# Optimization experiments

Measured on AMD Instinct MI355X. Metric: run time of the kernel, lower is better.

Reference implementation:

```python
import jax, jax.numpy as jnp
import numpy as np

B, S, E, H, W, L = 2048, 50, 256, 512, 256, 50  # batch, seq, emb, hidden, weight, answer_seq_len
V = 50 + 1  # input_size + 1 embedding rows


def _uni(k, shape, bound):
    return jax.random.uniform(k, shape, jnp.float32, -bound, bound)


def setup_inputs() -> dict:
    key = jax.random.key(0)
    ks = jax.random.split(key, 14)
    kb = 1.0 / np.sqrt(H)  # torch LSTM/Linear init bound 1/sqrt(hidden)
    inp = {
        'input': jax.random.randint(ks[0], (B, S), 0, V),
        'emb': jax.random.normal(ks[1], (V, E), jnp.float32),
        'enc_Wih': _uni(ks[2], (4 * H, E), kb),
        'enc_Whh': _uni(ks[3], (4 * H, H), kb),
        'enc_bih': _uni(ks[4], (4 * H,), kb),
        'enc_bhh': _uni(ks[5], (4 * H,), kb),
        'dec_Wih': _uni(ks[6], (4 * H, E), kb),
        'dec_Whh': _uni(ks[7], (4 * H, H), kb),
        'dec_bih': _uni(ks[8], (4 * H,), kb),
        'dec_bhh': _uni(ks[9], (4 * H,), kb),
        'W1': _uni(ks[10], (W, H), kb),
        'W2': _uni(ks[11], (W, H), kb),
        'vt': _uni(ks[12], (W,), 1.0 / np.sqrt(W)),
    }
    return inp


def _lstm_cell(x, h, c, Wih, Whh, bih, bhh):
    gates = x @ Wih.T + h @ Whh.T + (bih + bhh)
    i, f, g, o = jnp.split(gates, 4, axis=-1)  # torch gate order i,f,g,o
    c = jax.nn.sigmoid(f) * c + jax.nn.sigmoid(i) * jnp.tanh(g)
    h = jax.nn.sigmoid(o) * jnp.tanh(c)
    return h, c


def reference(input, emb, enc_Wih, enc_Whh, enc_bih, enc_bhh,
              dec_Wih, dec_Whh, dec_bih, dec_bhh, W1, W2, vt):
    x = emb[input]  # [B,S,E]

    def enc_step(carry, xt):
        h, c = carry
        h, c = _lstm_cell(xt, h, c, enc_Wih, enc_Whh, enc_bih, enc_bhh)
        return (h, c), h

    z = jnp.zeros((B, H), x.dtype)
    _, enc_seq = jax.lax.scan(enc_step, (z, z), x.transpose(1, 0, 2))  # [S,B,H]
    enc_states = enc_seq.transpose(1, 0, 2)  # [B,S,H]

    # W1(encoder_states) is loop-invariant; compute once (same math as per-step recompute)
    blend1 = jnp.einsum('bsh,wh->bsw', enc_states, W1)  # [B,S,W]

    dec_in = jnp.zeros((B, E), x.dtype)  # original never updates decoder_input
    h0 = jnp.zeros((B, H), x.dtype)
    c0 = enc_seq[-1]  # cell_state = encoder_states[-1]
    mask0 = jnp.zeros((B, S), bool)

    def dec_step(carry, k):
        h, c, mask = carry
        h, c = _lstm_cell(dec_in, h, c, dec_Wih, dec_Whh, dec_bih, dec_bhh)
        blend2 = h @ W2.T  # [B,W]
        scores = jnp.einsum('bsw,w->bs', jnp.tanh(blend1 + blend2[:, None, :]), vt)
        scores = jnp.where(mask, jnp.float32(-100000.0), scores)
        logp = jax.nn.log_softmax(scores, axis=-1)  # [B,S]
        chosen = jax.random.categorical(k, logp, axis=-1)  # [B]
        mask = mask.at[jnp.arange(B), chosen].set(True)
        return (h, c, mask), (logp, chosen)

    keys = jax.random.split(jax.random.key(42), L)
    _, (probs, tour) = jax.lax.scan(dec_step, (h0, c0, mask0), keys)
    probs = probs.transpose(1, 0, 2)  # [B,L,S]
    tour = tour.transpose(1, 0)       # [B,L]
    return probs, tour
```

## Files before the change

kernel.cpp:

```cpp
#include <hip/hip_runtime.h>
#include <cstdint>

#define Bsz 2048
#define Ssz 50
#define Esz 256
#define Hsz 512
#define Wsz 256
#define Lsz 50
#define Vsz 51
#define KI 16
#define CH 10
#define GFRAGC2 ((size_t)32 * 128 * 512)

#define JAX_THREEFRY_PARTITIONABLE 1

typedef _Float16 f16;
typedef _Float16 f16x8 __attribute__((ext_vector_type(8)));
typedef float f32x4 __attribute__((ext_vector_type(4)));

__host__ __device__ __forceinline__ void threefry2x32_hd(
    unsigned k0, unsigned k1, unsigned x0, unsigned x1,
    unsigned& o0, unsigned& o1) {
  unsigned ks2 = k0 ^ k1 ^ 0x1BD11BDAu;
  x0 += k0; x1 += k1;
#define TF_RND(r) { x0 += x1; x1 = (x1 << (r)) | (x1 >> (32 - (r))); x1 ^= x0; }
  TF_RND(13) TF_RND(15) TF_RND(26) TF_RND(6)
  x0 += k1; x1 += ks2 + 1u;
  TF_RND(17) TF_RND(29) TF_RND(16) TF_RND(24)
  x0 += ks2; x1 += k0 + 2u;
  TF_RND(13) TF_RND(15) TF_RND(26) TF_RND(6)
  x0 += k0; x1 += k1 + 3u;
  TF_RND(17) TF_RND(29) TF_RND(16) TF_RND(24)
  x0 += k1; x1 += ks2 + 4u;
  TF_RND(13) TF_RND(15) TF_RND(26) TF_RND(6)
  x0 += ks2; x1 += k0 + 5u;
#undef TF_RND
  o0 = x0; o1 = x1;
}

__global__ __launch_bounds__(512) void prep_gfrag(const float* __restrict__ Whh,
                                                  f16* __restrict__ dst) {
  int blk = blockIdx.x;
  int ntile = blk >> 5, kc = blk & 31;
  int t = threadIdx.x;
  int l = t >> 3, e = t & 7;
  int c = l & 15, kg = l >> 4;
  int n = ntile * 16 + c;
  int k = (kc & 15) * 32 + kg * 8 + e;
  int j = n >> 2, g = n & 3;
  float w = Whh[(size_t)(g * 512 + j) * 512 + k];
  f16 hi = (f16)w;
  float lo = w - (float)hi;
  f16 val = (kc < 16) ? hi : (f16)(lo * 2048.0f);
  dst[((size_t)kc * 128 + ntile) * 512 + t] = val;
}

__global__ __launch_bounds__(512) void prep_bfrag(const float* __restrict__ Wm,
                                                  f16* __restrict__ dst) {
  int blk = blockIdx.x;
  int wtile = blk >> 5, kc = blk & 31;
  int t = threadIdx.x;
  int l = t >> 3, e = t & 7;
  int c = l & 15, kg = l >> 4;
  int n = wtile * 16 + c;
  int k = (kc & 15) * 32 + kg * 8 + e;
  float w = Wm[(size_t)n * 512 + k];
  f16 hi = (f16)w;
  float lo = w - (float)hi;
  f16 val = (kc < 16) ? hi : (f16)(lo * 2048.0f);
  dst[((size_t)kc * 16 + wtile) * 512 + t] = val;
}

__global__ __launch_bounds__(256) void prep_encin(
    const float* __restrict__ emb, const float* __restrict__ Wih,
    const float* __restrict__ bih, const float* __restrict__ bhh,
    float* __restrict__ encInP) {
  int wid = blockIdx.x * 4 + (threadIdx.x >> 6);
  int lane = threadIdx.x & 63;
  if (wid >= Vsz * 2048) return;
  int v = wid >> 11, col = wid & 2047;
  float4 e = ((const float4*)emb)[v * 64 + lane];
  float4 w = ((const float4*)Wih)[col * 64 + lane];
  float d = e.x * w.x + e.y * w.y + e.z * w.z + e.w * w.w;
  for (int off = 32; off; off >>= 1) d += __shfl_xor(d, off);
  if (lane == 0) {
    int g = col >> 9, j = col & 511;
    encInP[(size_t)v * 2048 + j * 4 + g] = d + bih[col] + bhh[col];
  }
}

__global__ __launch_bounds__(256) void prep_dbias(const float* __restrict__ a,
                                                  const float* __restrict__ b,
                                                  float* __restrict__ dst) {
  int col = blockIdx.x * 256 + threadIdx.x;
  int g = col >> 9, j = col & 511;
  dst[j * 4 + g] = a[col] + b[col];
}

__global__ __launch_bounds__(256, 2) void gates_mfma(
    const f16* __restrict__ Afrag,
    const f16* __restrict__ Bfrag,
    const float* __restrict__ addtab, const int* __restrict__ input, int tstep,
    f16* __restrict__ Aout,
    float* __restrict__ cio) {
  __shared__ float Cst[64][132];
  const int t = threadIdx.x;
  const int lane = t & 63;
  const int wid = t >> 6;
  const int wm = wid >> 1, wn = wid & 1;
  const int bid = blockIdx.x;
  const int xcd = bid & 7, loc = bid >> 3;
  const int mblk = xcd * 4 + (loc >> 4);
  const int nblk = loc & 15;

  const f16* Ab = Afrag + (size_t)(mblk * 4 + wm * 2) * 512 + lane * 8;
  const f16* Bb = Bfrag + (size_t)(nblk * 8 + wn * 4) * 512 + lane * 8;

  f32x4 acc1[2][4], acc2[2][4];
  {
    f32x4 z = {0.f, 0.f, 0.f, 0.f};
#pragma unroll
    for (int i = 0; i < 2; ++i)
#pragma unroll
      for (int j = 0; j < 4; ++j) { acc1[i][j] = z; acc2[i][j] = z; }
  }

  f16x8 pah[2], pal[2], pbh[4], pbl[4];
  f16x8 qah[2], qal[2], qbh[4], qbl[4];

#define GLOAD(AH_, AL_, BH_, BL_, ki_)                                        \
  {                                                                           \
    const f16* ak = Ab + (size_t)(ki_)*65536;                                 \
    const f16* bk = Bb + (size_t)(ki_)*65536;                                 \
    _Pragma("unroll")                                                         \
    for (int q = 0; q < 2; ++q) {                                             \
      AH_[q] = *(const f16x8*)(ak + q * 512);                                 \
      AL_[q] = *(const f16x8*)(ak + (size_t)16 * 65536 + q * 512);            \
    }                                                                         \
    _Pragma("unroll")                                                         \
    for (int q = 0; q < 4; ++q) {                                             \
      BH_[q] = *(const f16x8*)(bk + q * 512);                                 \
      BL_[q] = *(const f16x8*)(bk + (size_t)16 * 65536 + q * 512);            \
    }                                                                         \
  }
#define GMM(AH_, AL_, BH_, BL_)                                               \
  {                                                                           \
    _Pragma("unroll")                                                         \
    for (int mt = 0; mt < 2; ++mt)                                            \
      _Pragma("unroll")                                                       \
      for (int nt = 0; nt < 4; ++nt)                                          \
        acc1[mt][nt] = __builtin_amdgcn_mfma_f32_16x16x32_f16(                \
            AH_[mt], BH_[nt], acc1[mt][nt], 0, 0, 0);                         \
    _Pragma("unroll")                                                         \
    for (int mt = 0; mt < 2; ++mt)                                            \
      _Pragma("unroll")                                                       \
      for (int nt = 0; nt < 4; ++nt)                                          \
        acc1[mt][nt] = __builtin_amdgcn_mfma_f32_16x16x32_f16(                \
            AL_[mt], BH_[nt], acc1[mt][nt], 0, 0, 0);                         \
    _Pragma("unroll")                                                         \
    for (int mt = 0; mt < 2; ++mt)                                            \
      _Pragma("unroll")                                                       \
      for (int nt = 0; nt < 4; ++nt)                                          \
        acc2[mt][nt] = __builtin_amdgcn_mfma_f32_16x16x32_f16(                \
            AH_[mt], BL_[nt], acc2[mt][nt], 0, 0, 0);                         \
  }

  GLOAD(pah, pal, pbh, pbl, 0)
#pragma unroll 1
  for (int ki = 0; ki < KI; ki += 2) {
    GLOAD(qah, qal, qbh, qbl, ki + 1)
    GMM(pah, pal, pbh, pbl)
    if (ki + 2 < KI) GLOAD(pah, pal, pbh, pbl, ki + 2)
    GMM(qah, qal, qbh, qbl)
  }
#undef GLOAD
#undef GMM

#pragma unroll
  for (int mt = 0; mt < 2; ++mt)
#pragma unroll
    for (int nt = 0; nt < 4; ++nt)
#pragma unroll
      for (int rg = 0; rg < 4; ++rg)
        Cst[wm * 32 + mt * 16 + (lane >> 4) * 4 + rg]
           [wn * 64 + nt * 16 + (lane & 15)] =
            acc1[mt][nt][rg] + acc2[mt][nt][rg] * (1.0f / 2048.0f);
  __syncthreads();

  const int bloc = t & 63, jg = t >> 6;
  const int bg = mblk * 64 + bloc;
  const float* arow = input
      ? addtab + (size_t)input[(size_t)bg * Ssz + tstep] * 2048
      : addtab;

  const int j0 = nblk * 32 + jg * 8;
  float* cp = cio + (size_t)bg * 512 + j0;
  float4 cv0 = *(const float4*)(cp);
  float4 cv1 = *(const float4*)(cp + 4);
  float cin[8] = {cv0.x, cv0.y, cv0.z, cv0.w, cv1.x, cv1.y, cv1.z, cv1.w};
  float cn[8], hv[8];
#pragma unroll
  for (int jj = 0; jj < 8; ++jj) {
    float4 gq = *(const float4*)(&Cst[bloc][jg * 32 + jj * 4]);
    float4 av = *(const float4*)(arow + (size_t)(j0 + jj) * 4);
    float gi = gq.x + av.x;
    float gf = gq.y + av.y;
    float gg = gq.z + av.z;
    float go = gq.w + av.w;
    float si = 1.0f / (1.0f + expf(-gi));
    float sf = 1.0f / (1.0f + expf(-gf));
    float sg = tanhf(gg);
    float so = 1.0f / (1.0f + expf(-go));
    float c2 = sf * cin[jj] + si * sg;
    cn[jj] = c2;
    hv[jj] = so * tanhf(c2);
  }
  *(float4*)(cp)     = make_float4(cn[0], cn[1], cn[2], cn[3]);
  *(float4*)(cp + 4) = make_float4(cn[4], cn[5], cn[6], cn[7]);

  f16x8 hi8, lo8;
#pragma unroll
  for (int jj = 0; jj < 8; ++jj) {
    f16 hi = (f16)hv[jj];
    hi8[jj] = hi;
    lo8[jj] = (f16)(hv[jj] - (float)hi);
  }
  const int kcH = j0 >> 5;
  const int kg = (j0 >> 3) & 3;
  size_t base = (((size_t)kcH * 128 + (bg >> 4)) * 64 + kg * 16 + (bg & 15)) * 8;
  *(f16x8*)(Aout + base)                       = hi8;
  *(f16x8*)(Aout + base + (size_t)16 * 65536)  = lo8;
}

__global__ __launch_bounds__(256) void blend_big(
    const f16* __restrict__ hChunk, const f16* __restrict__ Wb,
    float* __restrict__ outBase, int stepStride, int rowStride) {
  const int t = threadIdx.x, lane = t & 63, wid = t >> 6;
  const int wm = wid >> 1, wn = wid & 1;
  const int bid = blockIdx.x;
  const int xcd = bid & 7;
  const int r1 = bid >> 3;
  const int nblk = r1 & 7;
  const int r2 = r1 >> 3;
  const int mrem = r2 & 3;
  const int s = r2 >> 2;
  const int mblkL = xcd * 4 + mrem;
  const f16* Ab = hChunk + (size_t)s * GFRAGC2
                + (size_t)(mblkL * 4 + wm * 2) * 512 + lane * 8;
  const f16* Bb = Wb + (size_t)(nblk * 2 + wn) * 512 + lane * 8;

  f32x4 acc1[2], acc2[2];
  {
    f32x4 z = {0.f, 0.f, 0.f, 0.f};
    acc1[0] = z; acc1[1] = z; acc2[0] = z; acc2[1] = z;
  }
  f16x8 pah[2], pal[2], pbh, pbl, qah[2], qal[2], qbh, qbl;

#define BLOAD(AH_, AL_, BH_, BL_, ki_)                                        \
  {                                                                           \
    const f16* ak = Ab + (size_t)(ki_)*65536;                                 \
    const f16* bk = Bb + (size_t)(ki_)*8192;                                  \
    _Pragma("unroll")                                                         \
    for (int q = 0; q < 2; ++q) {                                             \
      AH_[q] = *(const f16x8*)(ak + q * 512);                                 \
      AL_[q] = *(const f16x8*)(ak + (size_t)16 * 65536 + q * 512);            \
    }                                                                         \
    BH_ = *(const f16x8*)(bk);                                                \
    BL_ = *(const f16x8*)(bk + (size_t)16 * 8192);                            \
  }
#define BMM(AH_, AL_, BH_, BL_)                                               \
  {                                                                           \
    _Pragma("unroll")                                                         \
    for (int mt = 0; mt < 2; ++mt)                                            \
      acc1[mt] = __builtin_amdgcn_mfma_f32_16x16x32_f16(                      \
          AH_[mt], BH_, acc1[mt], 0, 0, 0);                                   \
    _Pragma("unroll")                                                         \
    for (int mt = 0; mt < 2; ++mt)                                            \
      acc1[mt] = __builtin_amdgcn_mfma_f32_16x16x32_f16(                      \
          AL_[mt], BH_, acc1[mt], 0, 0, 0);                                   \
    _Pragma("unroll")                                                         \
    for (int mt = 0; mt < 2; ++mt)                                            \
      acc2[mt] = __builtin_amdgcn_mfma_f32_16x16x32_f16(                      \
          AH_[mt], BL_, acc2[mt], 0, 0, 0);                                   \
  }

  BLOAD(pah, pal, pbh, pbl, 0)
#pragma unroll 1
  for (int ki = 0; ki < KI; ki += 2) {
    BLOAD(qah, qal, qbh, qbl, ki + 1)
    BMM(pah, pal, pbh, pbl)
    if (ki + 2 < KI) BLOAD(pah, pal, pbh, pbl, ki + 2)
    BMM(qah, qal, qbh, qbl)
  }
#undef BLOAD
#undef BMM

  const int r = lane & 15, rg4 = (lane >> 4) * 4;
  float* ob = outBase + (size_t)s * stepStride;
#pragma unroll
  for (int mt = 0; mt < 2; ++mt)
#pragma unroll
    for (int rg = 0; rg < 4; ++rg) {
      int b = mblkL * 64 + wm * 32 + mt * 16 + rg4 + rg;
      int w = nblk * 32 + wn * 16 + r;
      float val = acc1[mt][rg] + acc2[mt][rg] * (1.0f / 2048.0f);
      ob[(size_t)b * rowStride + w] = __expf(2.0f * val);
    }
}

__global__ __launch_bounds__(256) void dec_cinit(const f16* __restrict__ hE,
                                                 float* __restrict__ cD) {
  int idx = blockIdx.x * 256 + threadIdx.x;
  int b = idx >> 9, j = idx & 511;
  size_t base = (((size_t)(j >> 5) * 128 + (b >> 4)) * 64
                 + ((j >> 3) & 3) * 16 + (b & 15)) * 8 + (j & 7);
  cD[idx] = (float)hE[base] + (float)hE[base + (size_t)16 * 65536];
}

__global__ __launch_bounds__(512) void sample_chunk(
    const float* __restrict__ b1, const float* __restrict__ b2c,
    const float* __restrict__ vt, unsigned long long* __restrict__ mask,
    float* __restrict__ probs, float* __restrict__ tour, int k0) {
  __shared__ float e1s[Ssz * Wsz];
  __shared__ float scbuf[2][52];
  const int t = threadIdx.x, b = blockIdx.x;
  const int wid = t >> 6, lane = t & 63;
  {
    const float4* src = (const float4*)(b1 + (size_t)b * Ssz * Wsz);
    for (int i = t; i < (Ssz * Wsz) / 4; i += 512)
      ((float4*)e1s)[i] = src[i];
  }
  const float vtr0 = vt[lane], vtr1 = vt[lane + 64];
  const float vtr2 = vt[lane + 128], vtr3 = vt[lane + 192];
  unsigned long long m = (wid == 7) ? mask[b] : 0ull;
  __syncthreads();

#define SCORE_ROWS(step_, dst_)                                               \
  {                                                                           \
    const float* b2p = b2c + ((size_t)(step_) * Bsz + b) * Wsz;               \
    float e20 = b2p[lane];                                                    \
    float e21 = b2p[lane + 64];                                               \
    float e22 = b2p[lane + 128];                                              \
    float e23 = b2p[lane + 192];                                              \
    for (int s = wid; s < Ssz; s += 7) {                                      \
      const float* row = e1s + s * Wsz;                                       \
      float r0 = __frcp_rn(fmaf(row[lane], e20, 1.0f));                       \
      float v = vtr0 * fmaf(-2.0f, r0, 1.0f);                                 \
      float r1 = __frcp_rn(fmaf(row[lane + 64], e21, 1.0f));                  \
      v += vtr1 * fmaf(-2.0f, r1, 1.0f);                                      \
      float r2 = __frcp_rn(fmaf(row[lane + 128], e22, 1.0f));                 \
      v += vtr2 * fmaf(-2.0f, r2, 1.0f);                                      \
      float r3 = __frcp_rn(fmaf(row[lane + 192], e23, 1.0f));                 \
      v += vtr3 * fmaf(-2.0f, r3, 1.0f);                                      \
      for (int off = 32; off; off >>= 1) v += __shfl_xor(v, off);             \
      if (lane == 0) (dst_)[s] = v;                                           \
    }                                                                         \
  }

  if (wid < 7) SCORE_ROWS(0, scbuf[0])
  __syncthreads();

#pragma unroll 1
  for (int kk = 0; kk < CH; ++kk) {
    if (wid < 7) {
      if (kk + 1 < CH) SCORE_ROWS(kk + 1, scbuf[(kk + 1) & 1])
    } else {
      const float* sc = scbuf[kk & 1];
      const int stepk = k0 + kk;
      float x = (lane < Ssz) ? sc[lane] : -INFINITY;
      if (lane < Ssz && ((m >> lane) & 1ull)) x = -100000.0f;
      float mv = x;
      for (int off = 32; off; off >>= 1) mv = fmaxf(mv, __shfl_xor(mv, off));
      float sh = x - mv;
      float e = (lane < Ssz) ? expf(sh) : 0.f;
      float ssum = e;
      for (int off = 32; off; off >>= 1) ssum += __shfl_xor(ssum, off);
      float lg = logf(ssum);
      float logp = sh - lg;
      if (lane < Ssz) probs[(size_t)b * (Lsz * Ssz) + stepk * Ssz + lane] = logp;

      unsigned kA, kB;
#if JAX_THREEFRY_PARTITIONABLE
      threefry2x32_hd(0u, 42u, 0u, (unsigned)stepk, kA, kB);
#else
      {
        unsigned a0, a1, c0, c1;
        int k = stepk;
        if (k < 25) {
          threefry2x32_hd(0u, 42u, 2u * k,      2u * k + 50u, a0, a1); kA = a0;
          threefry2x32_hd(0u, 42u, 2u * k + 1u, 2u * k + 51u, c0, c1); kB = c0;
        } else {
          threefry2x32_hd(0u, 42u, 2u * k - 50u, 2u * k,      a0, a1); kA = a1;
          threefry2x32_hd(0u, 42u, 2u * k - 49u, 2u * k + 1u, c0, c1); kB = c1;
        }
      }
#endif
      float val = -INFINITY;
      if (lane < Ssz) {
        unsigned j = (unsigned)(b * Ssz + lane);
        unsigned o0, o1, bits;
#if JAX_THREEFRY_PARTITIONABLE
        threefry2x32_hd(kA, kB, 0u, j, o0, o1);
        bits = o0 ^ o1;
#else
        if (j < 51200u) { threefry2x32_hd(kA, kB, j, j + 51200u, o0, o1); bits = o0; }
        else           { threefry2x32_hd(kA, kB, j - 51200u, j, o0, o1); bits = o1; }
#endif
        float f = __uint_as_float((bits >> 9) | 0x3F800000u) - 1.0f;
        float u = fmaxf(1.17549435e-38f, f + 1.17549435e-38f);
        val = logp - logf(-logf(u));
      }
      int idx = lane;
      for (int off = 32; off; off >>= 1) {
        float ov = __shfl_xor(val, off);
        int oi = __shfl_xor(idx, off);
        if (ov > val || (ov == val && oi < idx)) { val = ov; idx = oi; }
      }
      if (lane == 0) tour[(size_t)b * Lsz + stepk] = (float)idx;
      m |= (1ull << idx);
    }
    __syncthreads();
  }
#undef SCORE_ROWS
  if (wid == 7 && lane == 0) mask[b] = m;
}

extern "C" void kernel_launch(void* const* d_in, const int* in_sizes, int n_in,
                              void* d_out, int out_size, void* d_ws, size_t ws_size,
                              hipStream_t stream) {
  (void)in_sizes; (void)n_in; (void)out_size; (void)ws_size;
  const int*   input = (const int*)d_in[0];
  const float* emb   = (const float*)d_in[1];
  const float* eWih  = (const float*)d_in[2];
  const float* eWhh  = (const float*)d_in[3];
  const float* ebih  = (const float*)d_in[4];
  const float* ebhh  = (const float*)d_in[5];
  const float* dWhh  = (const float*)d_in[7];
  const float* dbih  = (const float*)d_in[8];
  const float* dbhh  = (const float*)d_in[9];
  const float* W1    = (const float*)d_in[10];
  const float* W2    = (const float*)d_in[11];
  const float* vt    = (const float*)d_in[12];
  float* outF = (float*)d_out;

  float* wsf = (float*)d_ws;
  size_t o = 0;
  const size_t BFRAG = (size_t)32 * 16 * 512;
  f16* BfE = (f16*)(wsf + o); o += GFRAGC2 / 2;
  f16* BfD = (f16*)(wsf + o); o += GFRAGC2 / 2;
  f16* Bb1 = (f16*)(wsf + o); o += BFRAG / 2;
  f16* Bb2 = (f16*)(wsf + o); o += BFRAG / 2;
  float* encInP = wsf + o; o += (size_t)Vsz * 2048;
  float* dbiasP = wsf + o; o += 2048;
  f16* hZero = (f16*)(wsf + o); o += GFRAGC2 / 2;
  f16* hBuf  = (f16*)(wsf + o); o += CH * (GFRAGC2 / 2);
  float* cE  = wsf + o; o += (size_t)Bsz * Hsz;
  float* b2c = wsf + o; o += (size_t)CH * Bsz * Wsz;
  float* b1  = wsf + o; o += (size_t)Bsz * Ssz * Wsz;
  unsigned long long* maskp = (unsigned long long*)(wsf + o); o += Bsz * 2;

  hipMemsetAsync(hZero, 0, GFRAGC2 * 2, stream);
  hipMemsetAsync(cE, 0, (size_t)Bsz * Hsz * 4, stream);
  hipMemsetAsync(maskp, 0, (size_t)Bsz * 8, stream);

  prep_gfrag<<<128 * 32, 512, 0, stream>>>(eWhh, BfE);
  prep_gfrag<<<128 * 32, 512, 0, stream>>>(dWhh, BfD);
  prep_bfrag<<<16 * 32, 512, 0, stream>>>(W1, Bb1);
  prep_bfrag<<<16 * 32, 512, 0, stream>>>(W2, Bb2);
  prep_encin<<<(Vsz * 2048) / 4, 256, 0, stream>>>(emb, eWih, ebih, ebhh, encInP);
  prep_dbias<<<8, 256, 0, stream>>>(dbih, dbhh, dbiasP);

  const size_t GF = GFRAGC2;

  for (int c = 0; c < Ssz / CH; ++c) {
    for (int s = 0; s < CH; ++s) {
      int t = c * CH + s;
      const f16* in = (t == 0) ? hZero : hBuf + (size_t)((t - 1) % CH) * GF;
      gates_mfma<<<512, 256, 0, stream>>>(in, BfE, encInP, input, t,
                                          hBuf + (size_t)s * GF, cE);
    }
    blend_big<<<8 * 8 * 4 * CH, 256, 0, stream>>>(hBuf, Bb1,
                                                  b1 + (size_t)(c * CH) * Wsz,
                                                  Wsz, Ssz * Wsz);
  }
  dec_cinit<<<(Bsz * Hsz) / 256, 256, 0, stream>>>(
      hBuf + (size_t)((Ssz - 1) % CH) * GF, cE);

  for (int c = 0; c < Lsz / CH; ++c) {
    for (int s = 0; s < CH; ++s) {
      int k = c * CH + s;
      const f16* in = (k == 0) ? hZero : hBuf + (size_t)((k - 1) % CH) * GF;
      gates_mfma<<<512, 256, 0, stream>>>(in, BfD, dbiasP, nullptr, 0,
                                          hBuf + (size_t)s * GF, cE);
    }
    blend_big<<<8 * 8 * 4 * CH, 256, 0, stream>>>(hBuf, Bb2, b2c,
                                                  Bsz * Wsz, Wsz);
    sample_chunk<<<Bsz, 512, 0, stream>>>(b1, b2c, vt, maskp, outF,
                                          outF + (size_t)Bsz * Lsz * Ssz,
                                          c * CH);
  }
}
```

Baseline: 3.289 ms.

## Fuse per-chunk LSTM gate steps into one persistent kernel with grid barrier

The ten per-step gates_mfma launches in each chunk become a single gates_chain launch. That kernel loops over the steps and synchronises all 512 blocks through a global atomic counter with spin-wait after each step. The counter is zeroed once and counts up across the encoder and decoder steps. The aim is to remove kernel launch and drain overhead between dependent recurrent steps, at the cost of a software grid barrier. This relies on all 512 blocks being co-resident, since the launch bounds allow two per CU, and it could deadlock if they are not.

```diff
diff --git a/kernel.cpp b/kernel.cpp
--- a/kernel.cpp
+++ b/kernel.cpp
@@ -97,12 +97,14 @@
   dst[j * 4 + g] = a[col] + b[col];
 }
 
-__global__ __launch_bounds__(256, 2) void gates_mfma(
-    const f16* __restrict__ Afrag,
+__global__ __launch_bounds__(256, 2) void gates_chain(
+    const f16* __restrict__ hIn0,
+    f16* __restrict__ hBuf,
     const f16* __restrict__ Bfrag,
-    const float* __restrict__ addtab, const int* __restrict__ input, int tstep,
-    f16* __restrict__ Aout,
-    float* __restrict__ cio) {
+    const float* __restrict__ addtab, const int* __restrict__ input,
+    int t0, int tzero,
+    float* __restrict__ cio,
+    unsigned* __restrict__ ctr) {
   __shared__ float Cst[64][132];
   const int t = threadIdx.x;
   const int lane = t & 63;
@@ -113,20 +115,27 @@
   const int mblk = xcd * 4 + (loc >> 4);
   const int nblk = loc & 15;
 
-  const f16* Ab = Afrag + (size_t)(mblk * 4 + wm * 2) * 512 + lane * 8;
+  const size_t aoff = (size_t)(mblk * 4 + wm * 2) * 512 + lane * 8;
   const f16* Bb = Bfrag + (size_t)(nblk * 8 + wn * 4) * 512 + lane * 8;
 
-  f32x4 acc1[2][4], acc2[2][4];
-  {
-    f32x4 z = {0.f, 0.f, 0.f, 0.f};
-#pragma unroll
-    for (int i = 0; i < 2; ++i)
-#pragma unroll
-      for (int j = 0; j < 4; ++j) { acc1[i][j] = z; acc2[i][j] = z; }
-  }
-
-  f16x8 pah[2], pal[2], pbh[4], pbl[4];
-  f16x8 qah[2], qal[2], qbh[4], qbl[4];
+#pragma unroll 1
+  for (int s = 0; s < CH; ++s) {
+    const int tstep = t0 + s;
+    const f16* Ab = ((tstep == tzero)
+                     ? hIn0 : hBuf + (size_t)((tstep - 1) % CH) * GFRAGC2) + aoff;
+    f16* Aout = hBuf + (size_t)(tstep % CH) * GFRAGC2;
+
+    f32x4 acc1[2][4], acc2[2][4];
+    {
+      f32x4 z = {0.f, 0.f, 0.f, 0.f};
+#pragma unroll
+      for (int i = 0; i < 2; ++i)
+#pragma unroll
+        for (int j = 0; j < 4; ++j) { acc1[i][j] = z; acc2[i][j] = z; }
+    }
+
+    f16x8 pah[2], pal[2], pbh[4], pbl[4];
+    f16x8 qah[2], qal[2], qbh[4], qbl[4];
 
 #define GLOAD(AH_, AL_, BH_, BL_, ki_)                                        \
   {                                                                           \
@@ -165,71 +174,85 @@
             AH_[mt], BL_[nt], acc2[mt][nt], 0, 0, 0);                         \
   }
 
-  GLOAD(pah, pal, pbh, pbl, 0)
+    GLOAD(pah, pal, pbh, pbl, 0)
 #pragma unroll 1
-  for (int ki = 0; ki < KI; ki += 2) {
-    GLOAD(qah, qal, qbh, qbl, ki + 1)
-    GMM(pah, pal, pbh, pbl)
-    if (ki + 2 < KI) GLOAD(pah, pal, pbh, pbl, ki + 2)
-    GMM(qah, qal, qbh, qbl)
-  }
+    for (int ki = 0; ki < KI; ki += 2) {
+      GLOAD(qah, qal, qbh, qbl, ki + 1)
+      GMM(pah, pal, pbh, pbl)
+      if (ki + 2 < KI) GLOAD(pah, pal, pbh, pbl, ki + 2)
+      GMM(qah, qal, qbh, qbl)
+    }
 #undef GLOAD
 #undef GMM
 
-#pragma unroll
-  for (int mt = 0; mt < 2; ++mt)
-#pragma unroll
-    for (int nt = 0; nt < 4; ++nt)
-#pragma unroll
-      for (int rg = 0; rg < 4; ++rg)
-        Cst[wm * 32 + mt * 16 + (lane >> 4) * 4 + rg]
-           [wn * 64 + nt * 16 + (lane & 15)] =
-            acc1[mt][nt][rg] + acc2[mt][nt][rg] * (1.0f / 2048.0f);
-  __syncthreads();
-
-  const int bloc = t & 63, jg = t >> 6;
-  const int bg = mblk * 64 + bloc;
-  const float* arow = input
-      ? addtab + (size_t)input[(size_t)bg * Ssz + tstep] * 2048
-      : addtab;
-
-  const int j0 = nblk * 32 + jg * 8;
-  float* cp = cio + (size_t)bg * 512 + j0;
-  float4 cv0 = *(const float4*)(cp);
-  float4 cv1 = *(const float4*)(cp + 4);
-  float cin[8] = {cv0.x, cv0.y, cv0.z, cv0.w, cv1.x, cv1.y, cv1.z, cv1.w};
-  float cn[8], hv[8];
-#pragma unroll
-  for (int jj = 0; jj < 8; ++jj) {
-    float4 gq = *(const float4*)(&Cst[bloc][jg * 32 + jj * 4]);
-    float4 av = *(const float4*)(arow + (size_t)(j0 + jj) * 4);
-    float gi = gq.x + av.x;
-    float gf = gq.y + av.y;
-    float gg = gq.z + av.z;
-    float go = gq.w + av.w;
-    float si = 1.0f / (1.0f + expf(-gi));
-    float sf = 1.0f / (1.0f + expf(-gf));
-    float sg = tanhf(gg);
-    float so = 1.0f / (1.0f + expf(-go));
-    float c2 = sf * cin[jj] + si * sg;
-    cn[jj] = c2;
-    hv[jj] = so * tanhf(c2);
-  }
-  *(float4*)(cp)     = make_float4(cn[0], cn[1], cn[2], cn[3]);
-  *(float4*)(cp + 4) = make_float4(cn[4], cn[5], cn[6], cn[7]);
-
-  f16x8 hi8, lo8;
-#pragma unroll
-  for (int jj = 0; jj < 8; ++jj) {
-    f16 hi = (f16)hv[jj];
-    hi8[jj] = hi;
-    lo8[jj] = (f16)(hv[jj] - (float)hi);
-  }
-  const int kcH = j0 >> 5;
-  const int kg = (j0 >> 3) & 3;
-  size_t base = (((size_t)kcH * 128 + (bg >> 4)) * 64 + kg * 16 + (bg & 15)) * 8;
-  *(f16x8*)(Aout + base)                       = hi8;
-  *(f16x8*)(Aout + base + (size_t)16 * 65536)  = lo8;
+    __syncthreads();
+#pragma unroll
+    for (int mt = 0; mt < 2; ++mt)
+#pragma unroll
+      for (int nt = 0; nt < 4; ++nt)
+#pragma unroll
+        for (int rg = 0; rg < 4; ++rg)
+          Cst[wm * 32 + mt * 16 + (lane >> 4) * 4 + rg]
+             [wn * 64 + nt * 16 + (lane & 15)] =
+              acc1[mt][nt][rg] + acc2[mt][nt][rg] * (1.0f / 2048.0f);
+    __syncthreads();
+
+    const int bloc = t & 63, jg = t >> 6;
+    const int bg = mblk * 64 + bloc;
+    const float* arow = input
+        ? addtab + (size_t)input[(size_t)bg * Ssz + tstep] * 2048
+        : addtab;
+
+    const int j0 = nblk * 32 + jg * 8;
+    float* cp = cio + (size_t)bg * 512 + j0;
+    float4 cv0 = *(const float4*)(cp);
+    float4 cv1 = *(const float4*)(cp + 4);
+    float cin[8] = {cv0.x, cv0.y, cv0.z, cv0.w, cv1.x, cv1.y, cv1.z, cv1.w};
+    float cn[8], hv[8];
+#pragma unroll
+    for (int jj = 0; jj < 8; ++jj) {
+      float4 gq = *(const float4*)(&Cst[bloc][jg * 32 + jj * 4]);
+      float4 av = *(const float4*)(arow + (size_t)(j0 + jj) * 4);
+      float gi = gq.x + av.x;
+      float gf = gq.y + av.y;
+      float gg = gq.z + av.z;
+      float go = gq.w + av.w;
+      float si = 1.0f / (1.0f + expf(-gi));
+      float sf = 1.0f / (1.0f + expf(-gf));
+      float sg = tanhf(gg);
+      float so = 1.0f / (1.0f + expf(-go));
+      float c2 = sf * cin[jj] + si * sg;
+      cn[jj] = c2;
+      hv[jj] = so * tanhf(c2);
+    }
+    *(float4*)(cp)     = make_float4(cn[0], cn[1], cn[2], cn[3]);
+    *(float4*)(cp + 4) = make_float4(cn[4], cn[5], cn[6], cn[7]);
+
+    f16x8 hi8, lo8;
+#pragma unroll
+    for (int jj = 0; jj < 8; ++jj) {
+      f16 hi = (f16)hv[jj];
+      hi8[jj] = hi;
+      lo8[jj] = (f16)(hv[jj] - (float)hi);
+    }
+    const int kcH = j0 >> 5;
+    const int kg = (j0 >> 3) & 3;
+    size_t base = (((size_t)kcH * 128 + (bg >> 4)) * 64 + kg * 16 + (bg & 15)) * 8;
+    *(f16x8*)(Aout + base)                       = hi8;
+    *(f16x8*)(Aout + base + (size_t)16 * 65536)  = lo8;
+
+    __syncthreads();
+    if (t == 0) {
+      __threadfence();
+      atomicAdd(ctr, 1u);
+      const unsigned target = (unsigned)(tstep + 1) * 512u;
+      while (__hip_atomic_load(ctr, __ATOMIC_RELAXED,
+                               __HIP_MEMORY_SCOPE_AGENT) < target)
+        __builtin_amdgcn_s_sleep(16);
+    }
+    __syncthreads();
+    __threadfence();
+  }
 }
 
 __global__ __launch_bounds__(256) void blend_big(
@@ -458,10 +481,12 @@
   float* b2c = wsf + o; o += (size_t)CH * Bsz * Wsz;
   float* b1  = wsf + o; o += (size_t)Bsz * Ssz * Wsz;
   unsigned long long* maskp = (unsigned long long*)(wsf + o); o += Bsz * 2;
+  unsigned* ctr = (unsigned*)(wsf + o); o += 64;
 
   hipMemsetAsync(hZero, 0, GFRAGC2 * 2, stream);
   hipMemsetAsync(cE, 0, (size_t)Bsz * Hsz * 4, stream);
   hipMemsetAsync(maskp, 0, (size_t)Bsz * 8, stream);
+  hipMemsetAsync(ctr, 0, 256, stream);
 
   prep_gfrag<<<128 * 32, 512, 0, stream>>>(eWhh, BfE);
   prep_gfrag<<<128 * 32, 512, 0, stream>>>(dWhh, BfD);
@@ -473,12 +498,8 @@
   const size_t GF = GFRAGC2;
 
   for (int c = 0; c < Ssz / CH; ++c) {
-    for (int s = 0; s < CH; ++s) {
-      int t = c * CH + s;
-      const f16* in = (t == 0) ? hZero : hBuf + (size_t)((t - 1) % CH) * GF;
-      gates_mfma<<<512, 256, 0, stream>>>(in, BfE, encInP, input, t,
-                                          hBuf + (size_t)s * GF, cE);
-    }
+    gates_chain<<<512, 256, 0, stream>>>(hZero, hBuf, BfE, encInP, input,
+                                         c * CH, 0, cE, ctr);
     blend_big<<<8 * 8 * 4 * CH, 256, 0, stream>>>(hBuf, Bb1,
                                                   b1 + (size_t)(c * CH) * Wsz,
                                                   Wsz, Ssz * Wsz);
@@ -487,12 +508,8 @@
       hBuf + (size_t)((Ssz - 1) % CH) * GF, cE);
 
   for (int c = 0; c < Lsz / CH; ++c) {
-    for (int s = 0; s < CH; ++s) {
-      int k = c * CH + s;
-      const f16* in = (k == 0) ? hZero : hBuf + (size_t)((k - 1) % CH) * GF;
-      gates_mfma<<<512, 256, 0, stream>>>(in, BfD, dbiasP, nullptr, 0,
-                                          hBuf + (size_t)s * GF, cE);
-    }
+    gates_chain<<<512, 256, 0, stream>>>(hZero, hBuf, BfD, dbiasP, nullptr,
+                                         Ssz + c * CH, Ssz, cE, ctr);
     blend_big<<<8 * 8 * 4 * CH, 256, 0, stream>>>(hBuf, Bb2, b2c,
                                                   Bsz * Wsz, Wsz);
     sample_chunk<<<Bsz, 512, 0, stream>>>(b1, b2c, vt, maskp, outF,
```

After: 11.87 ms. 261% more time.
